# Kernel optimization log

Measured on AMD Instinct MI355X. Metric: run time of the kernel, lower is better.

Reference implementation:

```python
import jax, jax.numpy as jnp
import numpy as np

B, L, D, H = 2, 2048, 1024, 16
HD = D // H  # head size = 64


def setup_inputs() -> dict:
    key = jax.random.key(0)
    ks = jax.random.split(key, 7)
    scale = 0.02
    return {
        "queries": jax.random.normal(ks[0], (B, L, D), dtype=jnp.float32),
        "keys": jax.random.normal(ks[1], (B, L, D), dtype=jnp.float32),
        "values": jax.random.normal(ks[2], (B, L, D), dtype=jnp.float32),
        "Wq": jax.random.normal(ks[3], (D, D), dtype=jnp.float32) * scale,
        "Wk": jax.random.normal(ks[4], (D, D), dtype=jnp.float32) * scale,
        "Wv": jax.random.normal(ks[5], (D, D), dtype=jnp.float32) * scale,
        "Wo": jax.random.normal(ks[6], (D, D), dtype=jnp.float32) * scale,
    }


def _split_heads(x):
    # (B, L, D) -> (B, H, L, HD); matches torch's transpose/view head split
    b, l, d = x.shape
    return x.reshape(b, l, H, HD).transpose(0, 2, 1, 3)


def reference(queries, keys, values, Wq, Wk, Wv, Wo):
    q = _split_heads(queries @ Wq.T)  # (B,H,Lq,HD)
    k = _split_heads(keys @ Wk.T)     # (B,H,Lk,HD)
    v = _split_heads(values @ Wv.T)   # (B,H,Lk,HD)

    scaling = jax.lax.rsqrt(jnp.float32(HD))
    scores = scaling * jnp.einsum("bhqd,bhkd->bhqk", q, k)  # (B,H,Lq,Lk)

    # Faithful to source quirk: mask = tril(scores); scores[mask == 0] = -inf.
    # This masks the strict upper triangle AND any lower-tri score exactly 0.
    tril_scores = jnp.tril(scores)
    scores = jnp.where(tril_scores == 0, -jnp.inf, scores)

    attention = jax.nn.softmax(scores, axis=-1)  # (B,H,Lq,Lk)

    context = jnp.einsum("bhqk,bhkd->bhqd", attention, v)  # (B,H,Lq,HD)
    context = context.transpose(0, 2, 1, 3).reshape(B, L, D)
    context = context @ Wo.T  # (B,Lq,D)
    return attention, context
```

## Files before the change

### kernel.cpp

```cpp
#include <hip/hip_runtime.h>
#include <hip/hip_bf16.h>

#define BB 2
#define LL 2048
#define DD 1024
#define HH 16
#define HDm 64
#define BHm 32

typedef __attribute__((ext_vector_type(8))) short short8;
typedef __attribute__((ext_vector_type(4))) float floatx4;

__device__ __forceinline__ unsigned short f2bf(float f) {
  union { float f; unsigned int u; } v; v.f = f;
  unsigned int r = v.u + 0x7fffu + ((v.u >> 16) & 1u);
  return (unsigned short)(r >> 16);
}

__device__ __forceinline__ short8 pack8(float4 a, float4 b) {
  short8 s;
  s[0]=(short)f2bf(a.x); s[1]=(short)f2bf(a.y); s[2]=(short)f2bf(a.z); s[3]=(short)f2bf(a.w);
  s[4]=(short)f2bf(b.x); s[5]=(short)f2bf(b.y); s[6]=(short)f2bf(b.z); s[7]=(short)f2bf(b.w);
  return s;
}

__global__ __launch_bounds__(256) void k_proj_qkv(
    const float* __restrict__ Xq, const float* __restrict__ Xk, const float* __restrict__ Xv,
    const float* __restrict__ Wq, const float* __restrict__ Wk, const float* __restrict__ Wv,
    unsigned short* __restrict__ Qh, unsigned short* __restrict__ Kh,
    unsigned short* __restrict__ Vt)
{
  const int which = blockIdx.z;
  const float* X = (which == 0) ? Xq : ((which == 1) ? Xk : Xv);
  const float* W = (which == 0) ? Wq : ((which == 1) ? Wk : Wv);

  const int I0 = blockIdx.x * 64;
  const int N0 = blockIdx.y * 64;
  const int tid = threadIdx.x;
  const int lane = tid & 63;
  const int w = tid >> 6;
  const int colb = lane & 15;
  const int rowb = (lane >> 4) * 4;
  const int kseg = (lane >> 4) * 8;

  __shared__ unsigned short Al[64 * 40];
  __shared__ unsigned short Bl[64 * 40];

  floatx4 acc[4] = {};
  const int sr = tid >> 2;
  const int sc = (tid & 3) * 8;

  for (int k0 = 0; k0 < DD; k0 += 32) {
    const float4* xa = reinterpret_cast<const float4*>(X + (size_t)(I0 + sr) * DD + k0 + sc);
    float4 a0 = xa[0], a1 = xa[1];
    const float4* xb = reinterpret_cast<const float4*>(W + (size_t)(N0 + sr) * DD + k0 + sc);
    float4 b0 = xb[0], b1 = xb[1];
    *reinterpret_cast<short8*>(&Al[sr * 40 + sc]) = pack8(a0, a1);
    *reinterpret_cast<short8*>(&Bl[sr * 40 + sc]) = pack8(b0, b1);
    __syncthreads();

    short8 af = *reinterpret_cast<const short8*>(&Al[(w * 16 + colb) * 40 + kseg]);
#pragma unroll
    for (int nt = 0; nt < 4; ++nt) {
      short8 bf = *reinterpret_cast<const short8*>(&Bl[(nt * 16 + colb) * 40 + kseg]);
      acc[nt] = __builtin_amdgcn_mfma_f32_16x16x32_bf16(af, bf, acc[nt], 0, 0, 0);
    }
    __syncthreads();
  }

#pragma unroll
  for (int nt = 0; nt < 4; ++nt) {
    int col = N0 + nt * 16 + colb;
    int h = col >> 6, hd = col & 63;
#pragma unroll
    for (int rr = 0; rr < 4; ++rr) {
      int row = I0 + w * 16 + rowb + rr;
      int b = row >> 11, l = row & 2047;
      unsigned short val = f2bf(acc[nt][rr]);
      if (which == 0)
        Qh[(((size_t)(b * HH + h)) * LL + l) * HDm + hd] = val;
      else if (which == 1)
        Kh[(((size_t)(b * HH + h)) * LL + l) * HDm + hd] = val;
      else
        Vt[(((size_t)(b * HH + h)) * HDm + hd) * LL + l] = val;
    }
  }
}

__global__ __launch_bounds__(256) void k_attn(
    const unsigned short* __restrict__ Qh,
    const unsigned short* __restrict__ Kh,
    const unsigned short* __restrict__ Vt,
    float* __restrict__ attn,
    unsigned short* __restrict__ Ctx)
{
  const int qt = blockIdx.x;
  const int bh = blockIdx.y;
  const int b = bh >> 4, h = bh & 15;
  const int Q0 = qt * 64;
  const int tid = threadIdx.x;
  const int lane = tid & 63;
  const int w = tid >> 6;
  const int colb = lane & 15;
  const int rowb = (lane >> 4) * 4;
  const int kseg = (lane >> 4) * 8;
  const float scale = 0.125f;

  __shared__ unsigned short Pl[64 * 72];

  const unsigned short* Qbase = Qh + (size_t)bh * LL * HDm;
  const unsigned short* Kbase = Kh + (size_t)bh * LL * HDm;
  const unsigned short* Vbase = Vt + (size_t)bh * HDm * LL;

  const int qrow = Q0 + w * 16 + colb;
  short8 qf0 = *reinterpret_cast<const short8*>(Qbase + (size_t)qrow * HDm + kseg);
  short8 qf1 = *reinterpret_cast<const short8*>(Qbase + (size_t)qrow * HDm + 32 + kseg);

  float m[4], ssum[4];
#pragma unroll
  for (int rr = 0; rr < 4; ++rr) { m[rr] = -__builtin_huge_valf(); ssum[rr] = 0.f; }

  for (int kt = 0; kt <= qt; ++kt) {
    const int K0 = kt * 64;
    floatx4 sacc[4] = {};
#pragma unroll
    for (int nt = 0; nt < 4; ++nt) {
      const unsigned short* kp = Kbase + (size_t)(K0 + nt * 16 + colb) * HDm + kseg;
      short8 kf0 = *reinterpret_cast<const short8*>(kp);
      short8 kf1 = *reinterpret_cast<const short8*>(kp + 32);
      sacc[nt] = __builtin_amdgcn_mfma_f32_16x16x32_bf16(qf0, kf0, sacc[nt], 0, 0, 0);
      sacc[nt] = __builtin_amdgcn_mfma_f32_16x16x32_bf16(qf1, kf1, sacc[nt], 0, 0, 0);
    }
#pragma unroll
    for (int rr = 0; rr < 4; ++rr) {
      int row = Q0 + w * 16 + rowb + rr;
      float v0, v1, v2, v3;
      {
        float sv = sacc[0][rr] * scale;
        v0 = ((K0 + 0 * 16 + colb) > row || sv == 0.0f) ? -__builtin_huge_valf() : sv;
        sv = sacc[1][rr] * scale;
        v1 = ((K0 + 1 * 16 + colb) > row || sv == 0.0f) ? -__builtin_huge_valf() : sv;
        sv = sacc[2][rr] * scale;
        v2 = ((K0 + 2 * 16 + colb) > row || sv == 0.0f) ? -__builtin_huge_valf() : sv;
        sv = sacc[3][rr] * scale;
        v3 = ((K0 + 3 * 16 + colb) > row || sv == 0.0f) ? -__builtin_huge_valf() : sv;
      }
      float tmax = fmaxf(fmaxf(v0, v1), fmaxf(v2, v3));
#pragma unroll
      for (int d = 1; d < 16; d <<= 1) tmax = fmaxf(tmax, __shfl_xor(tmax, d, 64));
      float mnew = fmaxf(m[rr], tmax);
      float psum = __expf(v0 - mnew) + __expf(v1 - mnew) + __expf(v2 - mnew) + __expf(v3 - mnew);
#pragma unroll
      for (int d = 1; d < 16; d <<= 1) psum += __shfl_xor(psum, d, 64);
      ssum[rr] = ssum[rr] * __expf(m[rr] - mnew) + psum;
      m[rr] = mnew;
    }
  }

  float inv[4];
#pragma unroll
  for (int rr = 0; rr < 4; ++rr) inv[rr] = 1.0f / ssum[rr];

  floatx4 cacc[4] = {};

  for (int kt = 0; kt <= qt; ++kt) {
    const int K0 = kt * 64;
    floatx4 sacc[4] = {};
#pragma unroll
    for (int nt = 0; nt < 4; ++nt) {
      const unsigned short* kp = Kbase + (size_t)(K0 + nt * 16 + colb) * HDm + kseg;
      short8 kf0 = *reinterpret_cast<const short8*>(kp);
      short8 kf1 = *reinterpret_cast<const short8*>(kp + 32);
      sacc[nt] = __builtin_amdgcn_mfma_f32_16x16x32_bf16(qf0, kf0, sacc[nt], 0, 0, 0);
      sacc[nt] = __builtin_amdgcn_mfma_f32_16x16x32_bf16(qf1, kf1, sacc[nt], 0, 0, 0);
    }
#pragma unroll
    for (int nt = 0; nt < 4; ++nt) {
      int col = K0 + nt * 16 + colb;
#pragma unroll
      for (int rr = 0; rr < 4; ++rr) {
        int row = Q0 + w * 16 + rowb + rr;
        float sv = sacc[nt][rr] * scale;
        bool masked = (col > row) || (sv == 0.0f);
        float p = masked ? 0.0f : __expf(sv - m[rr]) * inv[rr];
        attn[((size_t)bh * LL + row) * LL + col] = p;
        Pl[(w * 16 + rowb + rr) * 72 + nt * 16 + colb] = f2bf(p);
      }
    }
    __syncthreads();
#pragma unroll
    for (int s = 0; s < 2; ++s) {
      short8 pf = *reinterpret_cast<const short8*>(&Pl[(w * 16 + colb) * 72 + s * 32 + kseg]);
#pragma unroll
      for (int nt = 0; nt < 4; ++nt) {
        const unsigned short* vp = Vbase + (size_t)(nt * 16 + colb) * LL + K0 + s * 32 + kseg;
        short8 vf = *reinterpret_cast<const short8*>(vp);
        cacc[nt] = __builtin_amdgcn_mfma_f32_16x16x32_bf16(pf, vf, cacc[nt], 0, 0, 0);
      }
    }
    __syncthreads();
  }

  const int C0 = (qt + 1) * 64;
  if (C0 < LL) {
    const int zl4 = (LL - C0) >> 2;
    const float4 z = make_float4(0.f, 0.f, 0.f, 0.f);
    for (int row = 0; row < 64; ++row) {
      float4* dst = reinterpret_cast<float4*>(attn + ((size_t)bh * LL + Q0 + row) * LL + C0);
      for (int c = tid; c < zl4; c += 256) dst[c] = z;
    }
  }

#pragma unroll
  for (int nt = 0; nt < 4; ++nt) {
    int col = h * HDm + nt * 16 + colb;
#pragma unroll
    for (int rr = 0; rr < 4; ++rr) {
      int row = Q0 + w * 16 + rowb + rr;
      Ctx[((size_t)b * LL + row) * DD + col] = f2bf(cacc[nt][rr]);
    }
  }
}

__global__ __launch_bounds__(256) void k_out(
    const unsigned short* __restrict__ Ctx, const float* __restrict__ Wo,
    float* __restrict__ Out)
{
  const int I0 = blockIdx.x * 64;
  const int N0 = blockIdx.y * 64;
  const int tid = threadIdx.x;
  const int lane = tid & 63;
  const int w = tid >> 6;
  const int colb = lane & 15;
  const int rowb = (lane >> 4) * 4;
  const int kseg = (lane >> 4) * 8;

  __shared__ unsigned short Al[64 * 40];
  __shared__ unsigned short Bl[64 * 40];

  floatx4 acc[4] = {};
  const int sr = tid >> 2;
  const int sc = (tid & 3) * 8;

  for (int k0 = 0; k0 < DD; k0 += 32) {
    short8 av = *reinterpret_cast<const short8*>(Ctx + (size_t)(I0 + sr) * DD + k0 + sc);
    const float4* xb = reinterpret_cast<const float4*>(Wo + (size_t)(N0 + sr) * DD + k0 + sc);
    float4 b0 = xb[0], b1 = xb[1];
    *reinterpret_cast<short8*>(&Al[sr * 40 + sc]) = av;
    *reinterpret_cast<short8*>(&Bl[sr * 40 + sc]) = pack8(b0, b1);
    __syncthreads();

    short8 af = *reinterpret_cast<const short8*>(&Al[(w * 16 + colb) * 40 + kseg]);
#pragma unroll
    for (int nt = 0; nt < 4; ++nt) {
      short8 bf = *reinterpret_cast<const short8*>(&Bl[(nt * 16 + colb) * 40 + kseg]);
      acc[nt] = __builtin_amdgcn_mfma_f32_16x16x32_bf16(af, bf, acc[nt], 0, 0, 0);
    }
    __syncthreads();
  }

#pragma unroll
  for (int nt = 0; nt < 4; ++nt) {
    int col = N0 + nt * 16 + colb;
#pragma unroll
    for (int rr = 0; rr < 4; ++rr) {
      int row = I0 + w * 16 + rowb + rr;
      Out[(size_t)row * DD + col] = acc[nt][rr];
    }
  }
}

extern "C" void kernel_launch(void* const* d_in, const int* in_sizes, int n_in,
                              void* d_out, int out_size, void* d_ws, size_t ws_size,
                              hipStream_t stream) {
  const float* q  = (const float*)d_in[0];
  const float* k  = (const float*)d_in[1];
  const float* v  = (const float*)d_in[2];
  const float* wq = (const float*)d_in[3];
  const float* wk = (const float*)d_in[4];
  const float* wv = (const float*)d_in[5];
  const float* wo = (const float*)d_in[6];

  float* attn   = (float*)d_out;
  float* ctxout = (float*)d_out + (size_t)BHm * LL * LL;

  unsigned short* Qh  = (unsigned short*)d_ws;
  unsigned short* Kh  = Qh + (size_t)BHm * LL * HDm;
  unsigned short* Vt  = Kh + (size_t)BHm * LL * HDm;
  unsigned short* Ctx = Vt + (size_t)BHm * LL * HDm;

  k_proj_qkv<<<dim3(64, 16, 3), 256, 0, stream>>>(q, k, v, wq, wk, wv, Qh, Kh, Vt);
  k_attn<<<dim3(32, 32), 256, 0, stream>>>(Qh, Kh, Vt, attn, Ctx);
  k_out<<<dim3(64, 16), 256, 0, stream>>>(Ctx, wo, ctxout);
}
```

Baseline: 989.6 us.

## Pre-convert inputs to bf16, use LDS-direct GEMMs, fuse PV into first attention pass

A new kernel converts all fp32 inputs and weights to bf16 in workspace. A templated 128x64 GEMM then loads tiles straight into LDS with global_load_lds and serves both the projections and the output projection. The attention kernel now computes unnormalised exp(s) without a running max, accumulates P·V and the row sums (via MFMA against a ones vector) in the first pass, and writes Ctx right away. The second pass only recomputes probabilities and stores them with coalesced float4 writes staged through per-wave LDS. Dropping max subtraction risks overflow if scores grow large, and the conversion pass adds extra memory traffic.

```diff
diff --git a/kernel.cpp b/kernel.cpp
--- a/kernel.cpp
+++ b/kernel.cpp
@@ -1,15 +1,24 @@
 #include <hip/hip_runtime.h>
 #include <hip/hip_bf16.h>
 
-#define BB 2
 #define LL 2048
 #define DD 1024
 #define HH 16
-#define HDm 64
-#define BHm 32
 
 typedef __attribute__((ext_vector_type(8))) short short8;
 typedef __attribute__((ext_vector_type(4))) float floatx4;
+
+#define OFF_XQ 0ul
+#define OFF_XK 4194304ul
+#define OFF_XV 8388608ul
+#define OFF_WQ 12582912ul
+#define OFF_WK 13631488ul
+#define OFF_WV 14680064ul
+#define OFF_WO 15728640ul
+#define OFF_QH 16777216ul
+#define OFF_KH 20971520ul
+#define OFF_VT 25165824ul
+#define OFF_CT 29360128ul
 
 __device__ __forceinline__ unsigned short f2bf(float f) {
   union { float f; unsigned int u; } v; v.f = f;
@@ -24,65 +33,109 @@
   return s;
 }
 
-__global__ __launch_bounds__(256) void k_proj_qkv(
-    const float* __restrict__ Xq, const float* __restrict__ Xk, const float* __restrict__ Xv,
-    const float* __restrict__ Wq, const float* __restrict__ Wk, const float* __restrict__ Wv,
-    unsigned short* __restrict__ Qh, unsigned short* __restrict__ Kh,
-    unsigned short* __restrict__ Vt)
+#define GLOAD_LDS16(g, l)                                            \
+  __builtin_amdgcn_global_load_lds(                                  \
+      (const __attribute__((address_space(1))) void*)(g),            \
+      (__attribute__((address_space(3))) void*)(l), 16, 0, 0)
+
+__global__ __launch_bounds__(256) void k_cvt(
+    const float* __restrict__ x0, const float* __restrict__ x1, const float* __restrict__ x2,
+    const float* __restrict__ w0, const float* __restrict__ w1, const float* __restrict__ w2,
+    const float* __restrict__ w3, unsigned short* __restrict__ ws)
 {
-  const int which = blockIdx.z;
-  const float* X = (which == 0) ? Xq : ((which == 1) ? Xk : Xv);
-  const float* W = (which == 0) ? Wq : ((which == 1) ? Wk : Wv);
-
-  const int I0 = blockIdx.x * 64;
+  const int y = blockIdx.y;
+  const float* src; unsigned short* dst; int n;
+  switch (y) {
+    case 0: src = x0; dst = ws + OFF_XQ; n = 4194304; break;
+    case 1: src = x1; dst = ws + OFF_XK; n = 4194304; break;
+    case 2: src = x2; dst = ws + OFF_XV; n = 4194304; break;
+    case 3: src = w0; dst = ws + OFF_WQ; n = 1048576; break;
+    case 4: src = w1; dst = ws + OFF_WK; n = 1048576; break;
+    case 5: src = w2; dst = ws + OFF_WV; n = 1048576; break;
+    default: src = w3; dst = ws + OFF_WO; n = 1048576; break;
+  }
+  int i = (blockIdx.x * 256 + threadIdx.x) * 8;
+  if (i >= n) return;
+  const float4* p = reinterpret_cast<const float4*>(src + i);
+  *reinterpret_cast<short8*>(dst + i) = pack8(p[0], p[1]);
+}
+
+template<int MODE>
+__global__ __launch_bounds__(256) void k_gemm(
+    const unsigned short* __restrict__ A,
+    const unsigned short* __restrict__ B,
+    void* __restrict__ dstv)
+{
+  const int I0 = blockIdx.x * 128;
   const int N0 = blockIdx.y * 64;
   const int tid = threadIdx.x;
   const int lane = tid & 63;
   const int w = tid >> 6;
+  const int wr = w >> 1, wc = w & 1;
   const int colb = lane & 15;
   const int rowb = (lane >> 4) * 4;
   const int kseg = (lane >> 4) * 8;
 
-  __shared__ unsigned short Al[64 * 40];
-  __shared__ unsigned short Bl[64 * 40];
-
-  floatx4 acc[4] = {};
-  const int sr = tid >> 2;
-  const int sc = (tid & 3) * 8;
-
-  for (int k0 = 0; k0 < DD; k0 += 32) {
-    const float4* xa = reinterpret_cast<const float4*>(X + (size_t)(I0 + sr) * DD + k0 + sc);
-    float4 a0 = xa[0], a1 = xa[1];
-    const float4* xb = reinterpret_cast<const float4*>(W + (size_t)(N0 + sr) * DD + k0 + sc);
-    float4 b0 = xb[0], b1 = xb[1];
-    *reinterpret_cast<short8*>(&Al[sr * 40 + sc]) = pack8(a0, a1);
-    *reinterpret_cast<short8*>(&Bl[sr * 40 + sc]) = pack8(b0, b1);
+  __shared__ unsigned short Abuf[128 * 64];
+  __shared__ unsigned short Bbuf[64 * 64];
+
+  floatx4 acc[4][2] = {};
+
+  for (int k0 = 0; k0 < DD; k0 += 64) {
+#pragma unroll
+    for (int i = 0; i < 4; ++i) {
+      int e = (i * 4 + w) * 512 + lane * 8;
+      const unsigned short* g = A + (size_t)(I0 + (e >> 6)) * DD + k0 + (e & 63);
+      GLOAD_LDS16(g, Abuf + (i * 4 + w) * 512);
+    }
+#pragma unroll
+    for (int i = 0; i < 2; ++i) {
+      int e = (i * 4 + w) * 512 + lane * 8;
+      const unsigned short* g = B + (size_t)(N0 + (e >> 6)) * DD + k0 + (e & 63);
+      GLOAD_LDS16(g, Bbuf + (i * 4 + w) * 512);
+    }
     __syncthreads();
-
-    short8 af = *reinterpret_cast<const short8*>(&Al[(w * 16 + colb) * 40 + kseg]);
-#pragma unroll
-    for (int nt = 0; nt < 4; ++nt) {
-      short8 bf = *reinterpret_cast<const short8*>(&Bl[(nt * 16 + colb) * 40 + kseg]);
-      acc[nt] = __builtin_amdgcn_mfma_f32_16x16x32_bf16(af, bf, acc[nt], 0, 0, 0);
+#pragma unroll
+    for (int kk = 0; kk < 2; ++kk) {
+      short8 ar[4], br[2];
+#pragma unroll
+      for (int mi = 0; mi < 4; ++mi)
+        ar[mi] = *reinterpret_cast<const short8*>(
+            &Abuf[(wr * 64 + mi * 16 + colb) * 64 + kk * 32 + kseg]);
+#pragma unroll
+      for (int ni = 0; ni < 2; ++ni)
+        br[ni] = *reinterpret_cast<const short8*>(
+            &Bbuf[(wc * 32 + ni * 16 + colb) * 64 + kk * 32 + kseg]);
+#pragma unroll
+      for (int mi = 0; mi < 4; ++mi)
+#pragma unroll
+        for (int ni = 0; ni < 2; ++ni)
+          acc[mi][ni] = __builtin_amdgcn_mfma_f32_16x16x32_bf16(ar[mi], br[ni], acc[mi][ni], 0, 0, 0);
     }
     __syncthreads();
   }
 
 #pragma unroll
-  for (int nt = 0; nt < 4; ++nt) {
-    int col = N0 + nt * 16 + colb;
-    int h = col >> 6, hd = col & 63;
-#pragma unroll
-    for (int rr = 0; rr < 4; ++rr) {
-      int row = I0 + w * 16 + rowb + rr;
-      int b = row >> 11, l = row & 2047;
-      unsigned short val = f2bf(acc[nt][rr]);
-      if (which == 0)
-        Qh[(((size_t)(b * HH + h)) * LL + l) * HDm + hd] = val;
-      else if (which == 1)
-        Kh[(((size_t)(b * HH + h)) * LL + l) * HDm + hd] = val;
-      else
-        Vt[(((size_t)(b * HH + h)) * HDm + hd) * LL + l] = val;
+  for (int mi = 0; mi < 4; ++mi) {
+#pragma unroll
+    for (int ni = 0; ni < 2; ++ni) {
+      int col = N0 + wc * 32 + ni * 16 + colb;
+#pragma unroll
+      for (int rr = 0; rr < 4; ++rr) {
+        int row = I0 + wr * 64 + mi * 16 + rowb + rr;
+        if (MODE == 3) {
+          ((float*)dstv)[(size_t)row * DD + col] = acc[mi][ni][rr];
+        } else {
+          unsigned short val = f2bf(acc[mi][ni][rr]);
+          int h = col >> 6, hd = col & 63;
+          int b = row >> 11, l = row & 2047;
+          unsigned short* dst = (unsigned short*)dstv;
+          if (MODE == 0)
+            dst[(((size_t)(b * HH + h)) * LL + l) * 64 + hd] = val;
+          else
+            dst[(((size_t)(b * HH + h)) * 64 + hd) * LL + l] = val;
+        }
+      }
     }
   }
 }
@@ -106,69 +159,80 @@
   const int kseg = (lane >> 4) * 8;
   const float scale = 0.125f;
 
-  __shared__ unsigned short Pl[64 * 72];
-
-  const unsigned short* Qbase = Qh + (size_t)bh * LL * HDm;
-  const unsigned short* Kbase = Kh + (size_t)bh * LL * HDm;
-  const unsigned short* Vbase = Vt + (size_t)bh * HDm * LL;
+  __shared__ float Pf[4][16 * 68];
+  unsigned short* Plw = (unsigned short*)&Pf[w][0];
+  float* Pfw = &Pf[w][0];
+
+  const unsigned short* Qbase = Qh + (size_t)bh * LL * 64;
+  const unsigned short* Kbase = Kh + (size_t)bh * LL * 64;
+  const unsigned short* Vbase = Vt + (size_t)bh * 64 * LL;
 
   const int qrow = Q0 + w * 16 + colb;
-  short8 qf0 = *reinterpret_cast<const short8*>(Qbase + (size_t)qrow * HDm + kseg);
-  short8 qf1 = *reinterpret_cast<const short8*>(Qbase + (size_t)qrow * HDm + 32 + kseg);
-
-  float m[4], ssum[4];
-#pragma unroll
-  for (int rr = 0; rr < 4; ++rr) { m[rr] = -__builtin_huge_valf(); ssum[rr] = 0.f; }
+  short8 qf0 = *reinterpret_cast<const short8*>(Qbase + (size_t)qrow * 64 + kseg);
+  short8 qf1 = *reinterpret_cast<const short8*>(Qbase + (size_t)qrow * 64 + 32 + kseg);
+
+  short8 ones;
+#pragma unroll
+  for (int j = 0; j < 8; ++j) ones[j] = (short)0x3F80;
+
+  floatx4 ssum = {};
+  floatx4 cacc[4] = {};
 
   for (int kt = 0; kt <= qt; ++kt) {
     const int K0 = kt * 64;
     floatx4 sacc[4] = {};
 #pragma unroll
     for (int nt = 0; nt < 4; ++nt) {
-      const unsigned short* kp = Kbase + (size_t)(K0 + nt * 16 + colb) * HDm + kseg;
+      const unsigned short* kp = Kbase + (size_t)(K0 + nt * 16 + colb) * 64 + kseg;
       short8 kf0 = *reinterpret_cast<const short8*>(kp);
       short8 kf1 = *reinterpret_cast<const short8*>(kp + 32);
       sacc[nt] = __builtin_amdgcn_mfma_f32_16x16x32_bf16(qf0, kf0, sacc[nt], 0, 0, 0);
       sacc[nt] = __builtin_amdgcn_mfma_f32_16x16x32_bf16(qf1, kf1, sacc[nt], 0, 0, 0);
     }
 #pragma unroll
+    for (int nt = 0; nt < 4; ++nt) {
+      int col = K0 + nt * 16 + colb;
+#pragma unroll
+      for (int rr = 0; rr < 4; ++rr) {
+        int row = Q0 + w * 16 + rowb + rr;
+        float sv = sacc[nt][rr] * scale;
+        float e = ((col > row) || (sv == 0.0f)) ? 0.0f : __expf(sv);
+        Plw[(rowb + rr) * 72 + nt * 16 + colb] = f2bf(e);
+      }
+    }
+#pragma unroll
+    for (int s = 0; s < 2; ++s) {
+      short8 pf = *reinterpret_cast<const short8*>(&Plw[colb * 72 + s * 32 + kseg]);
+      ssum = __builtin_amdgcn_mfma_f32_16x16x32_bf16(pf, ones, ssum, 0, 0, 0);
+#pragma unroll
+      for (int nt = 0; nt < 4; ++nt) {
+        const unsigned short* vp = Vbase + (size_t)(nt * 16 + colb) * LL + K0 + s * 32 + kseg;
+        short8 vf = *reinterpret_cast<const short8*>(vp);
+        cacc[nt] = __builtin_amdgcn_mfma_f32_16x16x32_bf16(pf, vf, cacc[nt], 0, 0, 0);
+      }
+    }
+  }
+
+  float inv[4];
+#pragma unroll
+  for (int rr = 0; rr < 4; ++rr) inv[rr] = 1.0f / ssum[rr];
+
+#pragma unroll
+  for (int nt = 0; nt < 4; ++nt) {
+    int col = h * 64 + nt * 16 + colb;
+#pragma unroll
     for (int rr = 0; rr < 4; ++rr) {
       int row = Q0 + w * 16 + rowb + rr;
-      float v0, v1, v2, v3;
-      {
-        float sv = sacc[0][rr] * scale;
-        v0 = ((K0 + 0 * 16 + colb) > row || sv == 0.0f) ? -__builtin_huge_valf() : sv;
-        sv = sacc[1][rr] * scale;
-        v1 = ((K0 + 1 * 16 + colb) > row || sv == 0.0f) ? -__builtin_huge_valf() : sv;
-        sv = sacc[2][rr] * scale;
-        v2 = ((K0 + 2 * 16 + colb) > row || sv == 0.0f) ? -__builtin_huge_valf() : sv;
-        sv = sacc[3][rr] * scale;
-        v3 = ((K0 + 3 * 16 + colb) > row || sv == 0.0f) ? -__builtin_huge_valf() : sv;
-      }
-      float tmax = fmaxf(fmaxf(v0, v1), fmaxf(v2, v3));
-#pragma unroll
-      for (int d = 1; d < 16; d <<= 1) tmax = fmaxf(tmax, __shfl_xor(tmax, d, 64));
-      float mnew = fmaxf(m[rr], tmax);
-      float psum = __expf(v0 - mnew) + __expf(v1 - mnew) + __expf(v2 - mnew) + __expf(v3 - mnew);
-#pragma unroll
-      for (int d = 1; d < 16; d <<= 1) psum += __shfl_xor(psum, d, 64);
-      ssum[rr] = ssum[rr] * __expf(m[rr] - mnew) + psum;
-      m[rr] = mnew;
-    }
-  }
-
-  float inv[4];
-#pragma unroll
-  for (int rr = 0; rr < 4; ++rr) inv[rr] = 1.0f / ssum[rr];
-
-  floatx4 cacc[4] = {};
+      Ctx[((size_t)b * LL + row) * DD + col] = f2bf(cacc[nt][rr] * inv[rr]);
+    }
+  }
 
   for (int kt = 0; kt <= qt; ++kt) {
     const int K0 = kt * 64;
     floatx4 sacc[4] = {};
 #pragma unroll
     for (int nt = 0; nt < 4; ++nt) {
-      const unsigned short* kp = Kbase + (size_t)(K0 + nt * 16 + colb) * HDm + kseg;
+      const unsigned short* kp = Kbase + (size_t)(K0 + nt * 16 + colb) * 64 + kseg;
       short8 kf0 = *reinterpret_cast<const short8*>(kp);
       short8 kf1 = *reinterpret_cast<const short8*>(kp + 32);
       sacc[nt] = __builtin_amdgcn_mfma_f32_16x16x32_bf16(qf0, kf0, sacc[nt], 0, 0, 0);
@@ -181,24 +245,18 @@
       for (int rr = 0; rr < 4; ++rr) {
         int row = Q0 + w * 16 + rowb + rr;
         float sv = sacc[nt][rr] * scale;
-        bool masked = (col > row) || (sv == 0.0f);
-        float p = masked ? 0.0f : __expf(sv - m[rr]) * inv[rr];
-        attn[((size_t)bh * LL + row) * LL + col] = p;
-        Pl[(w * 16 + rowb + rr) * 72 + nt * 16 + colb] = f2bf(p);
-      }
-    }
-    __syncthreads();
-#pragma unroll
-    for (int s = 0; s < 2; ++s) {
-      short8 pf = *reinterpret_cast<const short8*>(&Pl[(w * 16 + colb) * 72 + s * 32 + kseg]);
-#pragma unroll
-      for (int nt = 0; nt < 4; ++nt) {
-        const unsigned short* vp = Vbase + (size_t)(nt * 16 + colb) * LL + K0 + s * 32 + kseg;
-        short8 vf = *reinterpret_cast<const short8*>(vp);
-        cacc[nt] = __builtin_amdgcn_mfma_f32_16x16x32_bf16(pf, vf, cacc[nt], 0, 0, 0);
-      }
-    }
-    __syncthreads();
+        float p = ((col > row) || (sv == 0.0f)) ? 0.0f : __expf(sv) * inv[rr];
+        Pfw[(rowb + rr) * 68 + nt * 16 + colb] = p;
+      }
+    }
+#pragma unroll
+    for (int i = 0; i < 4; ++i) {
+      int idx = i * 64 + lane;
+      int prow = idx >> 4, c4 = idx & 15;
+      float4 v = *reinterpret_cast<const float4*>(&Pfw[prow * 68 + c4 * 4]);
+      *reinterpret_cast<float4*>(
+          &attn[((size_t)bh * LL + Q0 + w * 16 + prow) * LL + K0 + c4 * 4]) = v;
+    }
   }
 
   const int C0 = (qt + 1) * 64;
@@ -208,64 +266,6 @@
     for (int row = 0; row < 64; ++row) {
       float4* dst = reinterpret_cast<float4*>(attn + ((size_t)bh * LL + Q0 + row) * LL + C0);
       for (int c = tid; c < zl4; c += 256) dst[c] = z;
-    }
-  }
-
-#pragma unroll
-  for (int nt = 0; nt < 4; ++nt) {
-    int col = h * HDm + nt * 16 + colb;
-#pragma unroll
-    for (int rr = 0; rr < 4; ++rr) {
-      int row = Q0 + w * 16 + rowb + rr;
-      Ctx[((size_t)b * LL + row) * DD + col] = f2bf(cacc[nt][rr]);
-    }
-  }
-}
-
-__global__ __launch_bounds__(256) void k_out(
-    const unsigned short* __restrict__ Ctx, const float* __restrict__ Wo,
-    float* __restrict__ Out)
-{
-  const int I0 = blockIdx.x * 64;
-  const int N0 = blockIdx.y * 64;
-  const int tid = threadIdx.x;
-  const int lane = tid & 63;
-  const int w = tid >> 6;
-  const int colb = lane & 15;
-  const int rowb = (lane >> 4) * 4;
-  const int kseg = (lane >> 4) * 8;
-
-  __shared__ unsigned short Al[64 * 40];
-  __shared__ unsigned short Bl[64 * 40];
-
-  floatx4 acc[4] = {};
-  const int sr = tid >> 2;
-  const int sc = (tid & 3) * 8;
-
-  for (int k0 = 0; k0 < DD; k0 += 32) {
-    short8 av = *reinterpret_cast<const short8*>(Ctx + (size_t)(I0 + sr) * DD + k0 + sc);
-    const float4* xb = reinterpret_cast<const float4*>(Wo + (size_t)(N0 + sr) * DD + k0 + sc);
-    float4 b0 = xb[0], b1 = xb[1];
-    *reinterpret_cast<short8*>(&Al[sr * 40 + sc]) = av;
-    *reinterpret_cast<short8*>(&Bl[sr * 40 + sc]) = pack8(b0, b1);
-    __syncthreads();
-
-    short8 af = *reinterpret_cast<const short8*>(&Al[(w * 16 + colb) * 40 + kseg]);
-#pragma unroll
-    for (int nt = 0; nt < 4; ++nt) {
-      short8 bf = *reinterpret_cast<const short8*>(&Bl[(nt * 16 + colb) * 40 + kseg]);
-      acc[nt] = __builtin_amdgcn_mfma_f32_16x16x32_bf16(af, bf, acc[nt], 0, 0, 0);
-    }
-    __syncthreads();
-  }
-
-#pragma unroll
-  for (int nt = 0; nt < 4; ++nt) {
-    int col = N0 + nt * 16 + colb;
-#pragma unroll
-    for (int rr = 0; rr < 4; ++rr) {
-      int row = I0 + w * 16 + rowb + rr;
-      Out[(size_t)row * DD + col] = acc[nt][rr];
     }
   }
 }
@@ -282,14 +282,14 @@
   const float* wo = (const float*)d_in[6];
 
   float* attn   = (float*)d_out;
-  float* ctxout = (float*)d_out + (size_t)BHm * LL * LL;
-
-  unsigned short* Qh  = (unsigned short*)d_ws;
-  unsigned short* Kh  = Qh + (size_t)BHm * LL * HDm;
-  unsigned short* Vt  = Kh + (size_t)BHm * LL * HDm;
-  unsigned short* Ctx = Vt + (size_t)BHm * LL * HDm;
-
-  k_proj_qkv<<<dim3(64, 16, 3), 256, 0, stream>>>(q, k, v, wq, wk, wv, Qh, Kh, Vt);
-  k_attn<<<dim3(32, 32), 256, 0, stream>>>(Qh, Kh, Vt, attn, Ctx);
-  k_out<<<dim3(64, 16), 256, 0, stream>>>(Ctx, wo, ctxout);
-}
+  float* ctxout = (float*)d_out + (size_t)32 * LL * LL;
+
+  unsigned short* ws = (unsigned short*)d_ws;
+
+  k_cvt<<<dim3(2048, 7), 256, 0, stream>>>(q, k, v, wq, wk, wv, wo, ws);
+  k_gemm<0><<<dim3(32, 16), 256, 0, stream>>>(ws + OFF_XQ, ws + OFF_WQ, ws + OFF_QH);
+  k_gemm<0><<<dim3(32, 16), 256, 0, stream>>>(ws + OFF_XK, ws + OFF_WK, ws + OFF_KH);
+  k_gemm<2><<<dim3(32, 16), 256, 0, stream>>>(ws + OFF_XV, ws + OFF_WV, ws + OFF_VT);
+  k_attn<<<dim3(32, 32), 256, 0, stream>>>(ws + OFF_QH, ws + OFF_KH, ws + OFF_VT, attn, ws + OFF_CT);
+  k_gemm<3><<<dim3(32, 16), 256, 0, stream>>>(ws + OFF_CT, ws + OFF_WO, ctxout);
+}
```

New measurement: 970.3 us. About the same (-2.0%).
